# Kernel optimization log

Hardware: AMD Instinct MI355X
Metric: run time of the kernel (lower is better)

Reference implementation:

```python
import jax, jax.numpy as jnp
import numpy as np

B, S, D, H, N = 1024, 2, 1, 128, 128  # batch, static_size, dynamic_size, hidden, num_nodes


def setup_inputs() -> dict:
    key = jax.random.key(0)
    ks = jax.random.split(key, 16)

    def xav(k, shape):
        fan = shape[0] + shape[1]
        lim = jnp.sqrt(6.0 / fan)
        return jax.random.uniform(k, shape, jnp.float32, -lim, lim)

    return {
        "static": jax.random.uniform(ks[0], (B, S, N), jnp.float32),
        "dynamic": jax.random.uniform(ks[1], (B, D, N), jnp.float32),
        # encoders (Conv1d kernel_size=1 == pointwise linear)
        "enc_s_w": xav(ks[2], (H, S)), "enc_s_b": jnp.zeros((H,), jnp.float32),
        "enc_d_w": xav(ks[3], (H, D)), "enc_d_b": jnp.zeros((H,), jnp.float32),
        # decoder params
        "x0": xav(ks[4], (1, S)),
        "emb_w": xav(ks[5], (H, S)), "emb_b": jnp.zeros((H,), jnp.float32),
        "w_ih": xav(ks[6], (3 * H, H)), "w_hh": xav(ks[7], (3 * H, H)),
        "b_ih": jnp.zeros((3 * H,), jnp.float32), "b_hh": jnp.zeros((3 * H,), jnp.float32),
        "attn_v": xav(ks[8], (1, H)), "attn_W": xav(ks[9], (H, 3 * H)),
        "dec_v": xav(ks[10], (1, H)), "dec_W": xav(ks[11], (H, 2 * H)),
    }


def _gru_cell(x, h, w_ih, w_hh, b_ih, b_hh):
    gi = x @ w_ih.T + b_ih  # [B, 3H]
    gh = h @ w_hh.T + b_hh
    i_r, i_z, i_n = jnp.split(gi, 3, axis=-1)
    h_r, h_z, h_n = jnp.split(gh, 3, axis=-1)
    r = jax.nn.sigmoid(i_r + h_r)
    z = jax.nn.sigmoid(i_z + h_z)
    n = jnp.tanh(i_n + r * h_n)
    return (1.0 - z) * n + z * h


def reference(static, dynamic, enc_s_w, enc_s_b, enc_d_w, enc_d_b, x0,
              emb_w, emb_b, w_ih, w_hh, b_ih, b_hh, attn_v, attn_W, dec_v, dec_W):
    # encoders: pointwise conv
    static_enc = jnp.einsum('hs,bsn->bhn', enc_s_w, static) + enc_s_b[None, :, None]
    dynamic_enc = jnp.einsum('hd,bdn->bhn', enc_d_w, dynamic) + enc_d_b[None, :, None]

    h0 = jnp.zeros((static.shape[0], H), jnp.float32)
    out0 = jnp.broadcast_to(x0, (static.shape[0], S))

    def step(carry, _):
        h, last_out = carry
        emb = last_out @ emb_w.T + emb_b                     # [B,H]
        h = _gru_cell(emb, h, w_ih, w_hh, b_ih, b_hh)        # [B,H]
        hid = jnp.broadcast_to(h[:, :, None], static_enc.shape)
        energy = jnp.concatenate([static_enc, dynamic_enc, hid], axis=1)   # [B,3H,N]
        u = jnp.tanh(jnp.einsum('hk,bkn->bhn', attn_W, energy))
        attn = jax.nn.softmax(jnp.einsum('h,bhn->bn', attn_v[0], u), axis=1)
        context = jnp.einsum('bn,bhn->bh', attn, static_enc)
        ctx = jnp.broadcast_to(context[:, :, None], static_enc.shape)
        energy2 = jnp.concatenate([static_enc, ctx], axis=1)               # [B,2H,N]
        u2 = jnp.tanh(jnp.einsum('hk,bkn->bhn', dec_W, energy2))
        logits = jnp.einsum('h,bhn->bn', dec_v[0], u2)
        probs = jax.nn.softmax(logits, axis=1)  # mask is all-ones -> log(mask)=0
        ptr = jnp.argmax(probs, axis=1)                       # [B]
        logp = jnp.log(jnp.max(probs, axis=1))
        last_out = jnp.take_along_axis(static, ptr[:, None, None], axis=2)[:, :, 0]
        return (h, last_out), (ptr, logp)

    (_, _), (ptrs, logps) = jax.lax.scan(step, (h0, out0), None, length=N)
    tour_idx = ptrs.T            # [B, N]
    tour_logp = logps.T.sum(axis=1)  # [B]
    return tour_idx, tour_logp
```

## Files before the change

kernel.cpp:

```cpp
#include <hip/hip_runtime.h>


#define H128 128
#define N128 128
#define B1024 1024
#define SC 2.885390081777927f

__device__ __forceinline__ float sigmoid_acc(float x){
    return 1.f / (1.f + expf(-x));
}
__device__ __forceinline__ float tanh_ps(float xs){
    float e = exp2f(xs);
    float r = __builtin_amdgcn_rcpf(e + 1.f);
    return fmaf(-2.f, r, 1.f);
}

__global__ void prep_kernel(const float* __restrict__ enc_s_w, const float* __restrict__ enc_s_b,
                            const float* __restrict__ enc_d_w, const float* __restrict__ enc_d_b,
                            const float* __restrict__ emb_w,   const float* __restrict__ emb_b,
                            const float* __restrict__ w_ih,    const float* __restrict__ b_ih,
                            const float* __restrict__ b_hh,
                            const float* __restrict__ attn_v,  const float* __restrict__ attn_W,
                            const float* __restrict__ dec_v,   const float* __restrict__ dec_W,
                            float4* __restrict__ A4, float4* __restrict__ D4,
                            float4* __restrict__ Q4, float4* __restrict__ G4)
{
    const int tid = threadIdx.x;
    const int blk = blockIdx.x;
    if (blk < 3){
        const int j = blk*128 + tid;
        const float* w = w_ih + j*H128;
        float a = 0.f, b = 0.f, c = 0.f;
        for (int k = 0; k < H128; ++k){
            float wv = w[k];
            a = fmaf(wv, emb_w[2*k],   a);
            b = fmaf(wv, emb_w[2*k+1], b);
            c = fmaf(wv, emb_b[k],     c);
        }
        G4[j] = make_float4(a, b, c + b_ih[j], b_hh[j]);
    } else {
        const int h = tid;
        const float* aw = attn_W + h*384;
        float u0=0.f, u1=0.f, u2=0.f, c1=0.f;
        for (int k = 0; k < H128; ++k){
            float w = aw[k];
            u0 = fmaf(w, enc_s_w[2*k],   u0);
            u1 = fmaf(w, enc_s_w[2*k+1], u1);
            c1 = fmaf(w, enc_s_b[k],     c1);
        }
        for (int k = 0; k < H128; ++k){
            float w = aw[128+k];
            u2 = fmaf(w, enc_d_w[k], u2);
            c1 = fmaf(w, enc_d_b[k], c1);
        }
        A4[h] = make_float4(SC*u0, SC*u1, SC*u2, attn_v[h]);
        const float* dw = dec_W + h*256;
        float v0=0.f, v1=0.f, c2=0.f, q0=0.f, q1=0.f;
        for (int k = 0; k < H128; ++k){
            float w = dw[k];
            v0 = fmaf(w, enc_s_w[2*k],   v0);
            v1 = fmaf(w, enc_s_w[2*k+1], v1);
            c2 = fmaf(w, enc_s_b[k],     c2);
        }
        for (int k = 0; k < H128; ++k){
            float w = dw[128+k];
            q0 = fmaf(w, enc_s_w[2*k],   q0);
            q1 = fmaf(w, enc_s_w[2*k+1], q1);
            c2 = fmaf(w, enc_s_b[k],     c2);
        }
        D4[h] = make_float4(SC*v0, SC*v1, dec_v[h], 0.f);
        Q4[h] = make_float4(SC*q0, SC*q1, SC*c2, SC*c1);
    }
}

__global__ void tp_kernel(const float* __restrict__ whh, const float* __restrict__ attnW,
                          float* __restrict__ WT, float* __restrict__ AT)
{
    const int idx = blockIdx.x*256 + threadIdx.x;
    if (idx < 49152){
        const int k = idx / 384, r = idx - k*384;
        WT[idx] = whh[r*H128 + k];
    } else {
        const int i2 = idx - 49152;
        const int k = i2 >> 7, j = i2 & 127;
        AT[i2] = SC * attnW[j*384 + 256 + k];
    }
}

__global__ __launch_bounds__(512, 4)
void decode_kernel(const float* __restrict__ statc, const float* __restrict__ dyn,
                   const float* __restrict__ x0,
                   const float* __restrict__ WT, const float* __restrict__ AT,
                   const float4* __restrict__ A4g, const float4* __restrict__ D4g,
                   const float4* __restrict__ Q4g, const float4* __restrict__ G4g,
                   float* __restrict__ out)
{
    __shared__ __align__(16) float hbuf[2][2][H128];
    __shared__ float gprz[2][2][256];
    __shared__ float gprn[2][4][H128];
    __shared__ float ahp[2][4][H128];
    __shared__ __align__(16) float ahl[2][H128];
    __shared__ __align__(16) float chl[2][H128];
    __shared__ float scp[2][2][H128];
    __shared__ float s0l[2][N128], s1l[2][N128];
    __shared__ float red[2][2][8];

    const int tid = threadIdx.x;
    const int mg  = tid >> 8;
    const int mn  = tid & 127;
    const int hi  = (tid >> 7) & 1;
    const int q   = (tid >> 7) & 3;
    const int rowa  = tid & 255;
    const int halfa = mg;
    const int b0  = blockIdx.x*2;

    const float s0n = statc[(b0+mg)*256 + mn];
    const float s1n = statc[(b0+mg)*256 + 128 + mn];
    const float d0n = dyn[(b0+mg)*128 + mn];
    s0l[mg][mn] = s0n; s1l[mg][mn] = s1n;

    const int cg = tid >> 7;
    const int cn = tid & 127;
    const int wvi = (tid >> 6) & 1;
    float4 Gr = make_float4(0,0,0,0), Gz = Gr, Gn = Gr, qv = Gr;
    float cs0n = 0.f, cs1n = 0.f, hreg = 0.f, lA = 0.f, lB = 0.f, logp = 0.f;
    if (tid < 256){
        Gr = G4g[cn]; Gz = G4g[128+cn]; Gn = G4g[256+cn];
        qv = Q4g[cn];
        cs0n = statc[(b0+cg)*256 + cn];
        cs1n = statc[(b0+cg)*256 + 128 + cn];
        hbuf[0][cg][cn] = 0.f;
        lA = x0[0]; lB = x0[1];
    }

    int cur = 0;
    __syncthreads();

    for (int t = 0; t < N128; ++t){
        const float4* h0v = (const float4*)&hbuf[cur][0][0];
        const float4* h1v = (const float4*)&hbuf[cur][1][0];
        {
            const float* pW = WT + rowa;
            float a0 = 0.f, a1 = 0.f;
            #pragma unroll 4
            for (int ki = 0; ki < 16; ++ki){
                const int k4 = halfa*16 + ki;
                float4 h0 = h0v[k4], h1 = h1v[k4];
                float w0 = pW[(4*k4+0)*384];
                float w1 = pW[(4*k4+1)*384];
                float w2 = pW[(4*k4+2)*384];
                float w3 = pW[(4*k4+3)*384];
                a0 = fmaf(w0,h0.x, fmaf(w1,h0.y, fmaf(w2,h0.z, fmaf(w3,h0.w, a0))));
                a1 = fmaf(w0,h1.x, fmaf(w1,h1.y, fmaf(w2,h1.z, fmaf(w3,h1.w, a1))));
            }
            gprz[0][halfa][rowa] = a0;
            gprz[1][halfa][rowa] = a1;
        }
        {
            const float* pW = WT + 256 + mn;
            float a0 = 0.f, a1 = 0.f;
            #pragma unroll 4
            for (int ki = 0; ki < 8; ++ki){
                const int k4 = q*8 + ki;
                float4 h0 = h0v[k4], h1 = h1v[k4];
                float w0 = pW[(4*k4+0)*384];
                float w1 = pW[(4*k4+1)*384];
                float w2 = pW[(4*k4+2)*384];
                float w3 = pW[(4*k4+3)*384];
                a0 = fmaf(w0,h0.x, fmaf(w1,h0.y, fmaf(w2,h0.z, fmaf(w3,h0.w, a0))));
                a1 = fmaf(w0,h1.x, fmaf(w1,h1.y, fmaf(w2,h1.z, fmaf(w3,h1.w, a1))));
            }
            gprn[0][q][mn] = a0;
            gprn[1][q][mn] = a1;
        }
        __syncthreads();
        if (tid < 256){
            float accr = gprz[cg][0][cn]     + gprz[cg][1][cn];
            float accz = gprz[cg][0][128+cn] + gprz[cg][1][128+cn];
            float accn = (gprn[cg][0][cn]+gprn[cg][1][cn]) + (gprn[cg][2][cn]+gprn[cg][3][cn]);
            float gir = fmaf(Gr.x, lA, fmaf(Gr.y, lB, Gr.z));
            float giz = fmaf(Gz.x, lA, fmaf(Gz.y, lB, Gz.z));
            float gin = fmaf(Gn.x, lA, fmaf(Gn.y, lB, Gn.z));
            float r  = sigmoid_acc(gir + (accr + Gr.w));
            float z  = sigmoid_acc(giz + (accz + Gz.w));
            float nn = tanhf(gin + r * (accn + Gn.w));
            float hnew = (1.f - z) * nn + z * hreg;
            hbuf[cur^1][cg][cn] = hnew; hreg = hnew;
        }
        __syncthreads();
        cur ^= 1;
        {
            const float4* hn0 = (const float4*)&hbuf[cur][0][0];
            const float4* hn1 = (const float4*)&hbuf[cur][1][0];
            const float* pA = AT + mn;
            float a0 = 0.f, a1 = 0.f;
            #pragma unroll 4
            for (int ki = 0; ki < 8; ++ki){
                const int k4 = q*8 + ki;
                float4 hv0 = hn0[k4], hv1 = hn1[k4];
                float w0 = pA[(4*k4+0)*128];
                float w1 = pA[(4*k4+1)*128];
                float w2 = pA[(4*k4+2)*128];
                float w3 = pA[(4*k4+3)*128];
                a0 = fmaf(w0,hv0.x, fmaf(w1,hv0.y, fmaf(w2,hv0.z, fmaf(w3,hv0.w, a0))));
                a1 = fmaf(w0,hv1.x, fmaf(w1,hv1.y, fmaf(w2,hv1.z, fmaf(w3,hv1.w, a1))));
            }
            ahp[0][q][mn] = a0;
            ahp[1][q][mn] = a1;
        }
        __syncthreads();
        if (tid < 256){
            ahl[cg][cn] = ((ahp[cg][0][cn]+ahp[cg][1][cn]) + (ahp[cg][2][cn]+ahp[cg][3][cn])) + qv.w;
        }
        __syncthreads();
        {
            const float4* ah4 = (const float4*)&ahl[mg][0];
            float sc = 0.f;
            #pragma unroll 2
            for (int kk = 0; kk < 16; ++kk){
                const int k = hi*16 + kk;
                float4 ah = ah4[k];
                { float4 a = A4g[4*k+0]; float tt = fmaf(a.x,s0n, fmaf(a.y,s1n, fmaf(a.z,d0n, ah.x))); sc = fmaf(tanh_ps(tt), a.w, sc); }
                { float4 a = A4g[4*k+1]; float tt = fmaf(a.x,s0n, fmaf(a.y,s1n, fmaf(a.z,d0n, ah.y))); sc = fmaf(tanh_ps(tt), a.w, sc); }
                { float4 a = A4g[4*k+2]; float tt = fmaf(a.x,s0n, fmaf(a.y,s1n, fmaf(a.z,d0n, ah.z))); sc = fmaf(tanh_ps(tt), a.w, sc); }
                { float4 a = A4g[4*k+3]; float tt = fmaf(a.x,s0n, fmaf(a.y,s1n, fmaf(a.z,d0n, ah.w))); sc = fmaf(tanh_ps(tt), a.w, sc); }
            }
            scp[mg][hi][mn] = sc;
        }
        __syncthreads();
        if (tid < 256){
            float sc = scp[cg][0][cn] + scp[cg][1][cn];
            float e  = __expf(sc);
            float se = e, sa = e * cs0n, sb = e * cs1n;
            #pragma unroll
            for (int off = 32; off > 0; off >>= 1){
                se += __shfl_xor(se, off, 64);
                sa += __shfl_xor(sa, off, 64);
                sb += __shfl_xor(sb, off, 64);
            }
            if ((tid & 63) == 0){ red[cg][wvi][0]=se; red[cg][wvi][1]=sa; red[cg][wvi][2]=sb; }
        }
        __syncthreads();
        if (tid < 256){
            float ssum = red[cg][0][0] + red[cg][1][0];
            float sat  = red[cg][0][1] + red[cg][1][1];
            float sbt  = red[cg][0][2] + red[cg][1][2];
            float cs0 = sat / ssum;
            float cs1 = sbt / ssum;
            chl[cg][cn] = fmaf(qv.x, cs0, fmaf(qv.y, cs1, qv.z));
        }
        __syncthreads();
        {
            const float4* ch4 = (const float4*)&chl[mg][0];
            float lg = 0.f;
            #pragma unroll 2
            for (int kk = 0; kk < 16; ++kk){
                const int k = hi*16 + kk;
                float4 ch = ch4[k];
                { float4 dd = D4g[4*k+0]; float tt = fmaf(dd.x,s0n, fmaf(dd.y,s1n, ch.x)); lg = fmaf(tanh_ps(tt), dd.z, lg); }
                { float4 dd = D4g[4*k+1]; float tt = fmaf(dd.x,s0n, fmaf(dd.y,s1n, ch.y)); lg = fmaf(tanh_ps(tt), dd.z, lg); }
                { float4 dd = D4g[4*k+2]; float tt = fmaf(dd.x,s0n, fmaf(dd.y,s1n, ch.z)); lg = fmaf(tanh_ps(tt), dd.z, lg); }
                { float4 dd = D4g[4*k+3]; float tt = fmaf(dd.x,s0n, fmaf(dd.y,s1n, ch.w)); lg = fmaf(tanh_ps(tt), dd.z, lg); }
            }
            scp[mg][hi][mn] = lg;
        }
        __syncthreads();
        if (tid < 256){
            float lg = scp[cg][0][cn] + scp[cg][1][cn];
            float v = lg; int bi = cn;
            #pragma unroll
            for (int off = 32; off > 0; off >>= 1){
                float ov = __shfl_xor(v, off, 64);
                int   oi = __shfl_xor(bi, off, 64);
                if (ov > v || (ov == v && oi < bi)){ v = ov; bi = oi; }
            }
            float e2 = __expf(lg - v);
            #pragma unroll
            for (int off = 32; off > 0; off >>= 1) e2 += __shfl_xor(e2, off, 64);
            if ((tid & 63) == 0){ red[cg][wvi][4]=v; red[cg][wvi][5]=__int_as_float(bi); red[cg][wvi][6]=e2; }
        }
        __syncthreads();
        if (tid < 256){
            float va = red[cg][0][4], vb = red[cg][1][4];
            int   ia = __float_as_int(red[cg][0][5]), ib = __float_as_int(red[cg][1][5]);
            float s2a = red[cg][0][6], s2b = red[cg][1][6];
            float m2; int ptr;
            if (va > vb || (va == vb && ia < ib)){ m2 = va; ptr = ia; } else { m2 = vb; ptr = ib; }
            float sum2 = fmaf(s2a, __expf(va - m2), s2b * __expf(vb - m2));
            logp -= logf(sum2);
            if (cn == 0) out[(b0+cg)*N128 + t] = (float)ptr;
            lA = s0l[cg][ptr];
            lB = s1l[cg][ptr];
        }
    }
    if (tid < 256 && cn == 0) out[B1024*N128 + (b0+cg)] = logp;
}

extern "C" void kernel_launch(void* const* d_in, const int* in_sizes, int n_in,
                              void* d_out, int out_size, void* d_ws, size_t ws_size,
                              hipStream_t stream)
{
    const float* statc   = (const float*)d_in[0];
    const float* dyn     = (const float*)d_in[1];
    const float* enc_s_w = (const float*)d_in[2];
    const float* enc_s_b = (const float*)d_in[3];
    const float* enc_d_w = (const float*)d_in[4];
    const float* enc_d_b = (const float*)d_in[5];
    const float* x0      = (const float*)d_in[6];
    const float* emb_w   = (const float*)d_in[7];
    const float* emb_b   = (const float*)d_in[8];
    const float* w_ih    = (const float*)d_in[9];
    const float* w_hh    = (const float*)d_in[10];
    const float* b_ih    = (const float*)d_in[11];
    const float* b_hh    = (const float*)d_in[12];
    const float* attn_v  = (const float*)d_in[13];
    const float* attn_W  = (const float*)d_in[14];
    const float* dec_v   = (const float*)d_in[15];
    const float* dec_W   = (const float*)d_in[16];

    float* ws = (float*)d_ws;
    float4* A4 = (float4*)(ws);
    float4* D4 = (float4*)(ws + 512);
    float4* Q4 = (float4*)(ws + 1024);
    float4* G4 = (float4*)(ws + 1536);
    float*  WT = ws + 3072;
    float*  AT = ws + 3072 + 49152;

    prep_kernel<<<dim3(4), dim3(128), 0, stream>>>(
        enc_s_w, enc_s_b, enc_d_w, enc_d_b, emb_w, emb_b,
        w_ih, b_ih, b_hh, attn_v, attn_W, dec_v, dec_W,
        A4, D4, Q4, G4);

    tp_kernel<<<dim3(256), dim3(256), 0, stream>>>(w_hh, attn_W, WT, AT);

    decode_kernel<<<dim3(B1024/2), dim3(512), 0, stream>>>(
        statc, dyn, x0, WT, AT,
        A4, D4, Q4, G4, (float*)d_out);
}
```

Baseline: 2.735 ms.

## Process four batch rows per block with weights held in registers

Each 512-thread block now decodes four batch elements instead of two, so every thread owns one (row, node) pair and the split-and-reduce passes for the attention and pointer scores go away, along with their barriers. The GRU and attention weight slices each thread needs (128 floats) are loaded once into registers before the time loop instead of being re-read from global memory every step. Each weight register is reused across four hidden-state vectors. In exchange, register pressure rises sharply (launch bounds lowered to 2 blocks per CU), and the grid halves to 256 blocks, which lowers occupancy and may underfill the GPU.

Measured after the change: 2.479 ms. 9.4% less time.

```diff
diff --git a/kernel.cpp b/kernel.cpp
--- a/kernel.cpp
+++ b/kernel.cpp
@@ -87,7 +87,7 @@
     }
 }
 
-__global__ __launch_bounds__(512, 4)
+__global__ __launch_bounds__(512, 2)
 void decode_kernel(const float* __restrict__ statc, const float* __restrict__ dyn,
                    const float* __restrict__ x0,
                    const float* __restrict__ WT, const float* __restrict__ AT,
@@ -95,43 +95,48 @@
                    const float4* __restrict__ Q4g, const float4* __restrict__ G4g,
                    float* __restrict__ out)
 {
-    __shared__ __align__(16) float hbuf[2][2][H128];
-    __shared__ float gprz[2][2][256];
-    __shared__ float gprn[2][4][H128];
-    __shared__ float ahp[2][4][H128];
-    __shared__ __align__(16) float ahl[2][H128];
-    __shared__ __align__(16) float chl[2][H128];
-    __shared__ float scp[2][2][H128];
-    __shared__ float s0l[2][N128], s1l[2][N128];
-    __shared__ float red[2][2][8];
+    __shared__ __align__(16) float hbuf[2][4][H128];
+    __shared__ float gprz[4][2][256];
+    __shared__ float gprn[4][4][H128];
+    __shared__ float ahp[4][4][H128];
+    __shared__ __align__(16) float ahl[4][H128];
+    __shared__ __align__(16) float chl[4][H128];
+    __shared__ float s0l[4][N128], s1l[4][N128];
+    __shared__ float red[4][2][8];
 
     const int tid = threadIdx.x;
-    const int mg  = tid >> 8;
-    const int mn  = tid & 127;
-    const int hi  = (tid >> 7) & 1;
-    const int q   = (tid >> 7) & 3;
+    const int cg    = tid >> 7;
+    const int cn    = tid & 127;
+    const int wvi   = (tid >> 6) & 1;
     const int rowa  = tid & 255;
-    const int halfa = mg;
-    const int b0  = blockIdx.x*2;
-
-    const float s0n = statc[(b0+mg)*256 + mn];
-    const float s1n = statc[(b0+mg)*256 + 128 + mn];
-    const float d0n = dyn[(b0+mg)*128 + mn];
-    s0l[mg][mn] = s0n; s1l[mg][mn] = s1n;
-
-    const int cg = tid >> 7;
-    const int cn = tid & 127;
-    const int wvi = (tid >> 6) & 1;
-    float4 Gr = make_float4(0,0,0,0), Gz = Gr, Gn = Gr, qv = Gr;
-    float cs0n = 0.f, cs1n = 0.f, hreg = 0.f, lA = 0.f, lB = 0.f, logp = 0.f;
-    if (tid < 256){
-        Gr = G4g[cn]; Gz = G4g[128+cn]; Gn = G4g[256+cn];
-        qv = Q4g[cn];
-        cs0n = statc[(b0+cg)*256 + cn];
-        cs1n = statc[(b0+cg)*256 + 128 + cn];
-        hbuf[0][cg][cn] = 0.f;
-        lA = x0[0]; lB = x0[1];
+    const int halfa = tid >> 8;
+    const int q     = cg;
+    const int b0    = blockIdx.x*4;
+
+    float wrz[64], wn[32], wa[32];
+    {
+        const float* pW = WT + rowa;
+        #pragma unroll
+        for (int j = 0; j < 64; ++j) wrz[j] = pW[(halfa*64 + j)*384];
+        const float* pN = WT + 256 + cn;
+        #pragma unroll
+        for (int j = 0; j < 32; ++j) wn[j] = pN[(q*32 + j)*384];
+        const float* pA = AT + cn;
+        #pragma unroll
+        for (int j = 0; j < 32; ++j) wa[j] = pA[(q*32 + j)*128];
     }
+
+    const float4 Gr = G4g[cn], Gz = G4g[128+cn], Gn = G4g[256+cn];
+    const float4 qv = Q4g[cn];
+
+    const float s0n = statc[(b0+cg)*256 + cn];
+    const float s1n = statc[(b0+cg)*256 + 128 + cn];
+    const float d0n = dyn[(b0+cg)*128 + cn];
+    s0l[cg][cn] = s0n; s1l[cg][cn] = s1n;
+    hbuf[0][cg][cn] = 0.f;
+    float hreg = 0.f;
+    float lA = x0[0], lB = x0[1];
+    float logp = 0.f;
 
     int cur = 0;
     __syncthreads();
@@ -139,42 +144,44 @@
     for (int t = 0; t < N128; ++t){
         const float4* h0v = (const float4*)&hbuf[cur][0][0];
         const float4* h1v = (const float4*)&hbuf[cur][1][0];
-        {
-            const float* pW = WT + rowa;
-            float a0 = 0.f, a1 = 0.f;
-            #pragma unroll 4
-            for (int ki = 0; ki < 16; ++ki){
-                const int k4 = halfa*16 + ki;
-                float4 h0 = h0v[k4], h1 = h1v[k4];
-                float w0 = pW[(4*k4+0)*384];
-                float w1 = pW[(4*k4+1)*384];
-                float w2 = pW[(4*k4+2)*384];
-                float w3 = pW[(4*k4+3)*384];
+        const float4* h2v = (const float4*)&hbuf[cur][2][0];
+        const float4* h3v = (const float4*)&hbuf[cur][3][0];
+        {
+            float a0=0.f, a1=0.f, a2=0.f, a3=0.f;
+            #pragma unroll
+            for (int j4 = 0; j4 < 16; ++j4){
+                const int k4 = halfa*16 + j4;
+                float4 h0 = h0v[k4], h1 = h1v[k4], h2 = h2v[k4], h3 = h3v[k4];
+                float w0 = wrz[4*j4+0], w1 = wrz[4*j4+1], w2 = wrz[4*j4+2], w3 = wrz[4*j4+3];
                 a0 = fmaf(w0,h0.x, fmaf(w1,h0.y, fmaf(w2,h0.z, fmaf(w3,h0.w, a0))));
                 a1 = fmaf(w0,h1.x, fmaf(w1,h1.y, fmaf(w2,h1.z, fmaf(w3,h1.w, a1))));
+                a2 = fmaf(w0,h2.x, fmaf(w1,h2.y, fmaf(w2,h2.z, fmaf(w3,h2.w, a2))));
+                a3 = fmaf(w0,h3.x, fmaf(w1,h3.y, fmaf(w2,h3.z, fmaf(w3,h3.w, a3))));
             }
             gprz[0][halfa][rowa] = a0;
             gprz[1][halfa][rowa] = a1;
-        }
-        {
-            const float* pW = WT + 256 + mn;
-            float a0 = 0.f, a1 = 0.f;
-            #pragma unroll 4
-            for (int ki = 0; ki < 8; ++ki){
-                const int k4 = q*8 + ki;
-                float4 h0 = h0v[k4], h1 = h1v[k4];
-                float w0 = pW[(4*k4+0)*384];
-                float w1 = pW[(4*k4+1)*384];
-                float w2 = pW[(4*k4+2)*384];
-                float w3 = pW[(4*k4+3)*384];
+            gprz[2][halfa][rowa] = a2;
+            gprz[3][halfa][rowa] = a3;
+        }
+        {
+            float a0=0.f, a1=0.f, a2=0.f, a3=0.f;
+            #pragma unroll
+            for (int j4 = 0; j4 < 8; ++j4){
+                const int k4 = q*8 + j4;
+                float4 h0 = h0v[k4], h1 = h1v[k4], h2 = h2v[k4], h3 = h3v[k4];
+                float w0 = wn[4*j4+0], w1 = wn[4*j4+1], w2 = wn[4*j4+2], w3 = wn[4*j4+3];
                 a0 = fmaf(w0,h0.x, fmaf(w1,h0.y, fmaf(w2,h0.z, fmaf(w3,h0.w, a0))));
                 a1 = fmaf(w0,h1.x, fmaf(w1,h1.y, fmaf(w2,h1.z, fmaf(w3,h1.w, a1))));
-            }
-            gprn[0][q][mn] = a0;
-            gprn[1][q][mn] = a1;
-        }
-        __syncthreads();
-        if (tid < 256){
+                a2 = fmaf(w0,h2.x, fmaf(w1,h2.y, fmaf(w2,h2.z, fmaf(w3,h2.w, a2))));
+                a3 = fmaf(w0,h3.x, fmaf(w1,h3.y, fmaf(w2,h3.z, fmaf(w3,h3.w, a3))));
+            }
+            gprn[0][q][cn] = a0;
+            gprn[1][q][cn] = a1;
+            gprn[2][q][cn] = a2;
+            gprn[3][q][cn] = a3;
+        }
+        __syncthreads();
+        {
             float accr = gprz[cg][0][cn]     + gprz[cg][1][cn];
             float accz = gprz[cg][0][128+cn] + gprz[cg][1][128+cn];
             float accn = (gprn[cg][0][cn]+gprn[cg][1][cn]) + (gprn[cg][2][cn]+gprn[cg][3][cn]);
@@ -190,48 +197,42 @@
         __syncthreads();
         cur ^= 1;
         {
-            const float4* hn0 = (const float4*)&hbuf[cur][0][0];
-            const float4* hn1 = (const float4*)&hbuf[cur][1][0];
-            const float* pA = AT + mn;
-            float a0 = 0.f, a1 = 0.f;
-            #pragma unroll 4
-            for (int ki = 0; ki < 8; ++ki){
-                const int k4 = q*8 + ki;
-                float4 hv0 = hn0[k4], hv1 = hn1[k4];
-                float w0 = pA[(4*k4+0)*128];
-                float w1 = pA[(4*k4+1)*128];
-                float w2 = pA[(4*k4+2)*128];
-                float w3 = pA[(4*k4+3)*128];
-                a0 = fmaf(w0,hv0.x, fmaf(w1,hv0.y, fmaf(w2,hv0.z, fmaf(w3,hv0.w, a0))));
-                a1 = fmaf(w0,hv1.x, fmaf(w1,hv1.y, fmaf(w2,hv1.z, fmaf(w3,hv1.w, a1))));
-            }
-            ahp[0][q][mn] = a0;
-            ahp[1][q][mn] = a1;
-        }
-        __syncthreads();
-        if (tid < 256){
-            ahl[cg][cn] = ((ahp[cg][0][cn]+ahp[cg][1][cn]) + (ahp[cg][2][cn]+ahp[cg][3][cn])) + qv.w;
-        }
-        __syncthreads();
-        {
-            const float4* ah4 = (const float4*)&ahl[mg][0];
+            const float4* n0 = (const float4*)&hbuf[cur][0][0];
+            const float4* n1 = (const float4*)&hbuf[cur][1][0];
+            const float4* n2 = (const float4*)&hbuf[cur][2][0];
+            const float4* n3 = (const float4*)&hbuf[cur][3][0];
+            float a0=0.f, a1=0.f, a2=0.f, a3=0.f;
+            #pragma unroll
+            for (int j4 = 0; j4 < 8; ++j4){
+                const int k4 = q*8 + j4;
+                float4 h0 = n0[k4], h1 = n1[k4], h2 = n2[k4], h3 = n3[k4];
+                float w0 = wa[4*j4+0], w1 = wa[4*j4+1], w2 = wa[4*j4+2], w3 = wa[4*j4+3];
+                a0 = fmaf(w0,h0.x, fmaf(w1,h0.y, fmaf(w2,h0.z, fmaf(w3,h0.w, a0))));
+                a1 = fmaf(w0,h1.x, fmaf(w1,h1.y, fmaf(w2,h1.z, fmaf(w3,h1.w, a1))));
+                a2 = fmaf(w0,h2.x, fmaf(w1,h2.y, fmaf(w2,h2.z, fmaf(w3,h2.w, a2))));
+                a3 = fmaf(w0,h3.x, fmaf(w1,h3.y, fmaf(w2,h3.z, fmaf(w3,h3.w, a3))));
+            }
+            ahp[0][q][cn] = a0;
+            ahp[1][q][cn] = a1;
+            ahp[2][q][cn] = a2;
+            ahp[3][q][cn] = a3;
+        }
+        __syncthreads();
+        ahl[cg][cn] = ((ahp[cg][0][cn]+ahp[cg][1][cn]) + (ahp[cg][2][cn]+ahp[cg][3][cn])) + qv.w;
+        __syncthreads();
+        {
+            const float4* ah4 = (const float4*)&ahl[cg][0];
             float sc = 0.f;
             #pragma unroll 2
-            for (int kk = 0; kk < 16; ++kk){
-                const int k = hi*16 + kk;
+            for (int k = 0; k < 32; ++k){
                 float4 ah = ah4[k];
                 { float4 a = A4g[4*k+0]; float tt = fmaf(a.x,s0n, fmaf(a.y,s1n, fmaf(a.z,d0n, ah.x))); sc = fmaf(tanh_ps(tt), a.w, sc); }
                 { float4 a = A4g[4*k+1]; float tt = fmaf(a.x,s0n, fmaf(a.y,s1n, fmaf(a.z,d0n, ah.y))); sc = fmaf(tanh_ps(tt), a.w, sc); }
                 { float4 a = A4g[4*k+2]; float tt = fmaf(a.x,s0n, fmaf(a.y,s1n, fmaf(a.z,d0n, ah.z))); sc = fmaf(tanh_ps(tt), a.w, sc); }
                 { float4 a = A4g[4*k+3]; float tt = fmaf(a.x,s0n, fmaf(a.y,s1n, fmaf(a.z,d0n, ah.w))); sc = fmaf(tanh_ps(tt), a.w, sc); }
             }
-            scp[mg][hi][mn] = sc;
-        }
-        __syncthreads();
-        if (tid < 256){
-            float sc = scp[cg][0][cn] + scp[cg][1][cn];
             float e  = __expf(sc);
-            float se = e, sa = e * cs0n, sb = e * cs1n;
+            float se = e, sa = e * s0n, sb = e * s1n;
             #pragma unroll
             for (int off = 32; off > 0; off >>= 1){
                 se += __shfl_xor(se, off, 64);
@@ -241,7 +242,7 @@
             if ((tid & 63) == 0){ red[cg][wvi][0]=se; red[cg][wvi][1]=sa; red[cg][wvi][2]=sb; }
         }
         __syncthreads();
-        if (tid < 256){
+        {
             float ssum = red[cg][0][0] + red[cg][1][0];
             float sat  = red[cg][0][1] + red[cg][1][1];
             float sbt  = red[cg][0][2] + red[cg][1][2];
@@ -251,22 +252,16 @@
         }
         __syncthreads();
         {
-            const float4* ch4 = (const float4*)&chl[mg][0];
+            const float4* ch4 = (const float4*)&chl[cg][0];
             float lg = 0.f;
             #pragma unroll 2
-            for (int kk = 0; kk < 16; ++kk){
-                const int k = hi*16 + kk;
+            for (int k = 0; k < 32; ++k){
                 float4 ch = ch4[k];
                 { float4 dd = D4g[4*k+0]; float tt = fmaf(dd.x,s0n, fmaf(dd.y,s1n, ch.x)); lg = fmaf(tanh_ps(tt), dd.z, lg); }
                 { float4 dd = D4g[4*k+1]; float tt = fmaf(dd.x,s0n, fmaf(dd.y,s1n, ch.y)); lg = fmaf(tanh_ps(tt), dd.z, lg); }
                 { float4 dd = D4g[4*k+2]; float tt = fmaf(dd.x,s0n, fmaf(dd.y,s1n, ch.z)); lg = fmaf(tanh_ps(tt), dd.z, lg); }
                 { float4 dd = D4g[4*k+3]; float tt = fmaf(dd.x,s0n, fmaf(dd.y,s1n, ch.w)); lg = fmaf(tanh_ps(tt), dd.z, lg); }
             }
-            scp[mg][hi][mn] = lg;
-        }
-        __syncthreads();
-        if (tid < 256){
-            float lg = scp[cg][0][cn] + scp[cg][1][cn];
             float v = lg; int bi = cn;
             #pragma unroll
             for (int off = 32; off > 0; off >>= 1){
@@ -280,7 +275,7 @@
             if ((tid & 63) == 0){ red[cg][wvi][4]=v; red[cg][wvi][5]=__int_as_float(bi); red[cg][wvi][6]=e2; }
         }
         __syncthreads();
-        if (tid < 256){
+        {
             float va = red[cg][0][4], vb = red[cg][1][4];
             int   ia = __float_as_int(red[cg][0][5]), ib = __float_as_int(red[cg][1][5]);
             float s2a = red[cg][0][6], s2b = red[cg][1][6];
@@ -293,7 +288,7 @@
             lB = s1l[cg][ptr];
         }
     }
-    if (tid < 256 && cn == 0) out[B1024*N128 + (b0+cg)] = logp;
+    if (cn == 0) out[B1024*N128 + (b0+cg)] = logp;
 }
 
 extern "C" void kernel_launch(void* const* d_in, const int* in_sizes, int n_in,
@@ -333,7 +328,7 @@
 
     tp_kernel<<<dim3(256), dim3(256), 0, stream>>>(w_hh, attn_W, WT, AT);
 
-    decode_kernel<<<dim3(B1024/2), dim3(512), 0, stream>>>(
+    decode_kernel<<<dim3(B1024/4), dim3(512), 0, stream>>>(
         statc, dyn, x0, WT, AT,
         A4, D4, Q4, G4, (float*)d_out);
 }
```
